# Optimization experiments

Hardware: AMD Instinct MI355X
Metric: run time of the kernel (lower is better)

The kernel has to match this reference:

```python
import jax, jax.numpy as jnp
import numpy as np

EPS = 1e-7  # keras K.epsilon()
ROUTINGS = 3


def squash(v, axis=-1):
    s = jnp.sum(v * v, axis=axis, keepdims=True)
    scale = s / (1.0 + s) / jnp.sqrt(s + EPS)
    return scale * v


def setup_inputs() -> dict:
    key = jax.random.key(0)
    k1, k2 = jax.random.split(key)
    B, I, K = 256, 2048, 8   # batch, input_num_capsule, input_dim_capsule
    J, D = 10, 16            # num_capsule, dim_capsule
    inputs = jax.random.normal(k1, (B, I, K), dtype=jnp.float32)
    W = jax.random.normal(k2, (J, I, D, K), dtype=jnp.float32) * 0.05
    return {"inputs": inputs, "W": W}


def reference(inputs, W):
    # inputs: [B, I, K]; W: [J, I, D, K]
    # inputs_hat[b,j,i,d] = W[j,i] @ inputs[b,i]  -> [B, J, I, D]
    u_hat = jnp.einsum('jidk,bik->bjid', W, inputs)
    B, J, I, _ = u_hat.shape
    b = jnp.zeros((B, J, 1, I), dtype=u_hat.dtype)
    outputs = None
    for r in range(ROUTINGS):
        c = jax.nn.softmax(b, axis=1)                       # softmax over output capsules
        s = jnp.einsum('bjqi,bjid->bjqd', c, u_hat)          # [B, J, 1, D]
        outputs = squash(s, axis=-1)
        if r < ROUTINGS - 1:
            b = b + jnp.einsum('bjqd,bjid->bjqi', outputs, u_hat)
    return jnp.squeeze(outputs, axis=2)                      # [B, J, D]
```

## Files before the change

### kernel.cpp

```cpp
#include <hip/hip_runtime.h>
#include <math.h>


#define BB 256
#define II 2048
#define KK 8
#define JJ 10
#define DD 16

typedef __attribute__((ext_vector_type(4))) float f32x4;
typedef __attribute__((ext_vector_type(8))) short short8;

__device__ __forceinline__ short f2bf(float f) {
    union { float f; unsigned u; } v; v.f = f;
    unsigned r = v.u + 0x7FFFu + ((v.u >> 16) & 1u);
    return (short)(r >> 16);
}

__global__ __launch_bounds__(256) void pre_kernel(const float* __restrict__ x,
                                                  const float* __restrict__ W,
                                                  short* __restrict__ xTb,
                                                  short* __restrict__ Wb) {
    __shared__ float4 tile[8 * 66];
    const int t = threadIdx.x;
    const int bid = blockIdx.x;
    if (bid < 1280) {
        const int idx = bid * 256 + t;
        const float4* src = (const float4*)(W + (size_t)idx * 8);
        const float4 a = src[0], b = src[1];
        short8 o;
        o[0] = f2bf(a.x); o[1] = f2bf(a.y); o[2] = f2bf(a.z); o[3] = f2bf(a.w);
        o[4] = f2bf(b.x); o[5] = f2bf(b.y); o[6] = f2bf(b.z); o[7] = f2bf(b.w);
        *(short8*)(Wb + (size_t)idx * 8) = o;
    } else {
        const int bb = bid - 1280;
        const int b0 = (bb >> 8) * 32, i0 = (bb & 255) * 8;
        {
            const int lb = t >> 3, li = t & 7;
            const float4* src = (const float4*)(x + ((b0 + lb) * II + (i0 + li)) * KK);
            tile[li * 66 + lb * 2 + 0] = src[0];
            tile[li * 66 + lb * 2 + 1] = src[1];
        }
        __syncthreads();
        {
            const int ri = t >> 5, rb = t & 31;
            const float4 p0 = tile[ri * 66 + rb * 2 + 0];
            const float4 p1 = tile[ri * 66 + rb * 2 + 1];
            short8 o;
            o[0] = f2bf(p0.x); o[1] = f2bf(p0.y); o[2] = f2bf(p0.z); o[3] = f2bf(p0.w);
            o[4] = f2bf(p1.x); o[5] = f2bf(p1.y); o[6] = f2bf(p1.z); o[7] = f2bf(p1.w);
            *(short8*)(xTb + ((size_t)(i0 + ri) * BB + (b0 + rb)) * KK) = o;
        }
    }
}

#define LBUF 14336

__device__ __forceinline__ void seg_src_dst(int s, int i0, int b0,
                                            const short* __restrict__ xTb,
                                            const short* __restrict__ Wb,
                                            const short** src, int* dst) {
    if (s < 20) {
        const int j = s >> 1, h = s & 1;
        *src = Wb + ((size_t)(j * II + i0) * DD) * KK + h * 512;
        *dst = j * 1024 + h * 512;
    } else {
        const int il = s - 20;
        *src = xTb + ((size_t)(i0 + il) * BB + b0) * KK;
        *dst = 10240 + il * 512;
    }
}

template <int USE_C>
__global__ __launch_bounds__(256) void round_mfma(
    const short* __restrict__ xTb, const short* __restrict__ Wb,
    const float* __restrict__ vT, _Float16* __restrict__ p)
{
    __shared__ short L[2][LBUF];
    const int t = threadIdx.x;
    const int lane = t & 63, wv = t >> 6;
    const int col = lane & 15, q = lane >> 4;
    const int b0 = blockIdx.y * 64;
    const int bl = wv * 16 + col;
    const int i0 = blockIdx.x * 16;

    short8 r0[7], r1[7];
#pragma unroll
    for (int n = 0; n < 7; ++n) {
        const int s = wv + n * 4;
        const short* src; int dst;
        seg_src_dst(s, i0, b0, xTb, Wb, &src, &dst);
        r0[n] = *(const short8*)(src + lane * 8);
        seg_src_dst(s, i0 + 8, b0, xTb, Wb, &src, &dst);
        r1[n] = *(const short8*)(src + lane * 8);
    }
#pragma unroll
    for (int n = 0; n < 7; ++n) {
        const int s = wv + n * 4;
        const short* src; int dst;
        seg_src_dst(s, i0, b0, xTb, Wb, &src, &dst);
        *(short8*)(&L[0][dst + lane * 8]) = r0[n];
    }
    __syncthreads();

    f32x4 sfrag[JJ];
#pragma unroll
    for (int j = 0; j < JJ; ++j) sfrag[j] = (f32x4){0.f, 0.f, 0.f, 0.f};

    float vfrag[JJ][4];
    if (USE_C) {
#pragma unroll
        for (int j = 0; j < JJ; ++j)
#pragma unroll
            for (int r = 0; r < 4; ++r)
                vfrag[j][r] = vT[(j * DD + q * 4 + r) * BB + b0 + bl];
    }

#pragma unroll
    for (int sc = 0; sc < 2; ++sc) {
        const short* Lb = L[sc];
        if (USE_C) {
            for (int il = 0; il < 8; ++il) {
                short8 A[JJ], Bf;
                const short8 z = (short8){0, 0, 0, 0, 0, 0, 0, 0};
                Bf = z;
#pragma unroll
                for (int j = 0; j < JJ; ++j) A[j] = z;
                if (q == 0) {
                    Bf = *(const short8*)(&Lb[10240 + il * 512 + bl * 8]);
#pragma unroll
                    for (int j = 0; j < JJ; ++j)
                        A[j] = *(const short8*)(&Lb[j * 1024 + il * 128 + col * 8]);
                }
                f32x4 U[JJ];
#pragma unroll
                for (int j = 0; j < JJ; ++j)
                    U[j] = __builtin_amdgcn_mfma_f32_16x16x32_bf16(
                        A[j], Bf, (f32x4){0.f, 0.f, 0.f, 0.f}, 0, 0, 0);
                float Lg[JJ];
#pragma unroll
                for (int j = 0; j < JJ; ++j)
                    Lg[j] = vfrag[j][0] * U[j][0] + vfrag[j][1] * U[j][1]
                          + vfrag[j][2] * U[j][2] + vfrag[j][3] * U[j][3];
#pragma unroll
                for (int j = 0; j < JJ; ++j) {
                    Lg[j] += __shfl_xor(Lg[j], 16, 64);
                    Lg[j] += __shfl_xor(Lg[j], 32, 64);
                }
                float sum = 0.f;
#pragma unroll
                for (int j = 0; j < JJ; ++j) { Lg[j] = __expf(Lg[j]); sum += Lg[j]; }
                const float inv = __builtin_amdgcn_rcpf(sum);
#pragma unroll
                for (int j = 0; j < JJ; ++j) {
                    const float c = Lg[j] * inv;
#pragma unroll
                    for (int r = 0; r < 4; ++r) sfrag[j][r] += c * U[j][r];
                }
            }
        } else {
#pragma unroll
            for (int s = 0; s < 2; ++s) {
                const int il = s * 4 + q;
                const short8 Bf = *(const short8*)(&Lb[10240 + il * 512 + bl * 8]);
#pragma unroll
                for (int j = 0; j < JJ; ++j) {
                    const short8 A = *(const short8*)(&Lb[j * 1024 + il * 128 + col * 8]);
                    sfrag[j] = __builtin_amdgcn_mfma_f32_16x16x32_bf16(A, Bf, sfrag[j], 0, 0, 0);
                }
            }
        }
        if (sc == 0) {
#pragma unroll
            for (int n = 0; n < 7; ++n) {
                const int s = wv + n * 4;
                const short* src; int dst;
                seg_src_dst(s, i0 + 8, b0, xTb, Wb, &src, &dst);
                *(short8*)(&L[1][dst + lane * 8]) = r1[n];
            }
            __syncthreads();
        }
    }

    _Float16* pp = p + ((size_t)(blockIdx.y * 4 + wv) * 128 + blockIdx.x) * (JJ * 256);
#pragma unroll
    for (int j = 0; j < JJ; ++j) {
        union { uint2 u; _Float16 h[4]; } pk;
        pk.h[0] = (_Float16)sfrag[j][0];
        pk.h[1] = (_Float16)sfrag[j][1];
        pk.h[2] = (_Float16)sfrag[j][2];
        pk.h[3] = (_Float16)sfrag[j][3];
        *(uint2*)(pp + (size_t)(j * 64 + lane) * 4) = pk.u;
    }
}

template <int MODE>
__global__ __launch_bounds__(256) void rs_kernel(const _Float16* __restrict__ p,
                                                 float* __restrict__ vT,
                                                 float* __restrict__ out, float scale) {
    __shared__ f32x4 red[256];
    const int t = threadIdx.x;
    const int j = blockIdx.x, bt = blockIdx.y;
    const int eg = t & 63, cg = t >> 6;

    const _Float16* pp = p + ((size_t)bt * 128 + cg * 32) * (JJ * 256) + j * 256 + eg * 4;
    float s0 = 0.f, s1 = 0.f, s2 = 0.f, s3 = 0.f;
#pragma unroll 8
    for (int ch = 0; ch < 32; ++ch) {
        union { uint2 u; _Float16 h[4]; } cv;
        cv.u = *(const uint2*)(pp + (size_t)ch * (JJ * 256));
        s0 += (float)cv.h[0]; s1 += (float)cv.h[1];
        s2 += (float)cv.h[2]; s3 += (float)cv.h[3];
    }
    red[t] = (f32x4){s0, s1, s2, s3};
    __syncthreads();
    if (t < 64) {
        f32x4 a = red[t];
        a += red[64 + t]; a += red[128 + t]; a += red[192 + t];
        const float x0 = a[0] * scale, x1 = a[1] * scale;
        const float x2 = a[2] * scale, x3 = a[3] * scale;
        float ss = x0 * x0 + x1 * x1 + x2 * x2 + x3 * x3;
        ss += __shfl_xor(ss, 16, 64);
        ss += __shfl_xor(ss, 32, 64);
        const float coef = ss / (1.f + ss) / sqrtf(ss + 1e-7f);
        const int qd = t >> 4, bc = t & 15;
        const float v[4] = {coef * x0, coef * x1, coef * x2, coef * x3};
#pragma unroll
        for (int r = 0; r < 4; ++r) {
            const int d = qd * 4 + r;
            if (MODE == 0) vT[(j * DD + d) * BB + bt * 16 + bc] = v[r];
            if (MODE == 1) vT[(j * DD + d) * BB + bt * 16 + bc] += v[r];
            if (MODE == 2) out[((bt * 16 + bc) * JJ + j) * DD + d] = v[r];
        }
    }
}

#define IT_OLD 32
#define BT_OLD 16

__global__ __launch_bounds__(256) void zero_kernel(float* __restrict__ p, int n) {
    int idx = blockIdx.x * blockDim.x + threadIdx.x;
    if (idx < n) p[idx] = 0.f;
}

__global__ __launch_bounds__(256) void squash_old(float* __restrict__ s_acc,
                                                  float* __restrict__ dst, float scale,
                                                  int add_to_dst, int zero_src) {
    int idx = blockIdx.x * blockDim.x + threadIdx.x;
    if (idx >= BB * JJ) return;
    float s[DD];
    float ss = 0.f;
#pragma unroll
    for (int d = 0; d < DD; ++d) {
        s[d] = s_acc[idx * DD + d] * scale;
        ss += s[d] * s[d];
    }
    const float coef = ss / (1.f + ss) / sqrtf(ss + 1e-7f);
#pragma unroll
    for (int d = 0; d < DD; ++d) {
        const float vv = coef * s[d];
        if (add_to_dst) dst[idx * DD + d] += vv;
        else            dst[idx * DD + d] = vv;
        if (zero_src)   s_acc[idx * DD + d] = 0.f;
    }
}

__global__ __launch_bounds__(256) void round1_old(const float* __restrict__ x,
                                                  const float* __restrict__ W,
                                                  float* __restrict__ s_acc) {
    const int t = threadIdx.x;
    const int d = t & 15;
    const int bq = t >> 4;
    const int b = blockIdx.y * BT_OLD + bq;
    const int i0 = blockIdx.x * IT_OLD;
    float acc[JJ];
#pragma unroll
    for (int j = 0; j < JJ; ++j) acc[j] = 0.f;
    for (int ii = 0; ii < IT_OLD; ++ii) {
        const int i = i0 + ii;
        const float* xp = x + ((b * II) + i) * KK;
        const float4 xa = *(const float4*)(xp);
        const float4 xb = *(const float4*)(xp + 4);
#pragma unroll
        for (int j = 0; j < JJ; ++j) {
            const float* wp = W + (((j * II + i) * DD + d) * KK);
            const float4 w0 = *(const float4*)(wp);
            const float4 w1 = *(const float4*)(wp + 4);
            acc[j] += w0.x*xa.x + w0.y*xa.y + w0.z*xa.z + w0.w*xa.w
                    + w1.x*xb.x + w1.y*xb.y + w1.z*xb.z + w1.w*xb.w;
        }
    }
#pragma unroll
    for (int j = 0; j < JJ; ++j)
        atomicAdd(&s_acc[(b * JJ + j) * DD + d], acc[j]);
}

__global__ __launch_bounds__(256) void round_old(const float* __restrict__ x,
                                                 const float* __restrict__ W,
                                                 const float* __restrict__ v,
                                                 float* __restrict__ s_acc) {
    const int t = threadIdx.x;
    const int d = t & 15;
    const int bq = t >> 4;
    const int b = blockIdx.y * BT_OLD + bq;
    const int i0 = blockIdx.x * IT_OLD;
    float vr[JJ], acc[JJ];
#pragma unroll
    for (int j = 0; j < JJ; ++j) {
        vr[j] = v[(b * JJ + j) * DD + d];
        acc[j] = 0.f;
    }
    for (int ii = 0; ii < IT_OLD; ++ii) {
        const int i = i0 + ii;
        const float* xp = x + ((b * II) + i) * KK;
        const float4 xa = *(const float4*)(xp);
        const float4 xb = *(const float4*)(xp + 4);
        float U[JJ], Lg[JJ];
#pragma unroll
        for (int j = 0; j < JJ; ++j) {
            const float* wp = W + (((j * II + i) * DD + d) * KK);
            const float4 w0 = *(const float4*)(wp);
            const float4 w1 = *(const float4*)(wp + 4);
            U[j] = w0.x*xa.x + w0.y*xa.y + w0.z*xa.z + w0.w*xa.w
                 + w1.x*xb.x + w1.y*xb.y + w1.z*xb.z + w1.w*xb.w;
            Lg[j] = vr[j] * U[j];
        }
#pragma unroll
        for (int m = 8; m >= 1; m >>= 1) {
#pragma unroll
            for (int j = 0; j < JJ; ++j) Lg[j] += __shfl_xor(Lg[j], m, 64);
        }
        float mx = Lg[0];
#pragma unroll
        for (int j = 1; j < JJ; ++j) mx = fmaxf(mx, Lg[j]);
        float sum = 0.f;
#pragma unroll
        for (int j = 0; j < JJ; ++j) { Lg[j] = __expf(Lg[j] - mx); sum += Lg[j]; }
        const float inv = 1.f / sum;
#pragma unroll
        for (int j = 0; j < JJ; ++j) acc[j] += (Lg[j] * inv) * U[j];
    }
#pragma unroll
    for (int j = 0; j < JJ; ++j)
        atomicAdd(&s_acc[(b * JJ + j) * DD + d], acc[j]);
}

extern "C" void kernel_launch(void* const* d_in, const int* in_sizes, int n_in,
                              void* d_out, int out_size, void* d_ws, size_t ws_size,
                              hipStream_t stream) {
    const float* x = (const float*)d_in[0];
    const float* W = (const float*)d_in[1];
    float* out = (float*)d_out;

    float* vT     = (float*)d_ws;
    _Float16* p   = (_Float16*)(vT + BB * JJ * DD);
    short* xTb    = (short*)(p + (size_t)16 * 128 * 2560);
    short* Wb     = xTb + (size_t)II * BB * KK;
    const size_t need = (size_t)(BB * JJ * DD) * 4
                      + (size_t)16 * 128 * 2560 * 2
                      + ((size_t)II * BB * KK + (size_t)JJ * II * DD * KK) * 2;

    if (ws_size >= need) {
        pre_kernel<<<1280 + 2048, 256, 0, stream>>>(x, W, xTb, Wb);

        dim3 rg(128, 4);
        dim3 sg(JJ, 16);
        round_mfma<0><<<rg, 256, 0, stream>>>(xTb, Wb, vT, p);
        rs_kernel<0><<<sg, 256, 0, stream>>>(p, vT, out, 0.1f);
        round_mfma<1><<<rg, 256, 0, stream>>>(xTb, Wb, vT, p);
        rs_kernel<1><<<sg, 256, 0, stream>>>(p, vT, out, 1.0f);
        round_mfma<1><<<rg, 256, 0, stream>>>(xTb, Wb, vT, p);
        rs_kernel<2><<<sg, 256, 0, stream>>>(p, vT, out, 1.0f);
    } else {
        float* s_acc = (float*)d_ws;
        float* v_buf = s_acc + BB * JJ * DD;
        const int NS = BB * JJ * DD;
        dim3 rg(II / IT_OLD, BB / BT_OLD);
        zero_kernel<<<(NS + 255) / 256, 256, 0, stream>>>(s_acc, NS);
        round1_old<<<rg, 256, 0, stream>>>(x, W, s_acc);
        squash_old<<<(BB * JJ + 255) / 256, 256, 0, stream>>>(s_acc, v_buf, 0.1f, 0, 1);
        round_old<<<rg, 256, 0, stream>>>(x, W, v_buf, s_acc);
        squash_old<<<(BB * JJ + 255) / 256, 256, 0, stream>>>(s_acc, v_buf, 1.0f, 1, 1);
        round_old<<<rg, 256, 0, stream>>>(x, W, v_buf, s_acc);
        squash_old<<<(BB * JJ + 255) / 256, 256, 0, stream>>>(s_acc, out, 1.0f, 0, 0);
    }
}
```

Measured before the change: 139.9 us.

## Double the input-capsule chunk per block with pipelined loads and packed partial sums

Each round_mfma block now covers 32 input capsules in four 8-capsule stages instead of 16 in two. Global loads for stage n+2 are issued while stage n is computed, and LDS buffers alternate between stages. Block IDs are remapped so that neighbouring blocks share W chunks across batch tiles. The partial-sum buffer is halved, its layout packs two output capsules per 16-byte store, and vT is changed to a [j][b][d] layout so it can be read with vector loads; rs_kernel is rewritten to match. The grid drops to 256 blocks, which lowers parallelism and may hurt occupancy across the GPU's compute units.

```diff
diff --git a/kernel.cpp b/kernel.cpp
--- a/kernel.cpp
+++ b/kernel.cpp
@@ -80,26 +80,29 @@
     const int t = threadIdx.x;
     const int lane = t & 63, wv = t >> 6;
     const int col = lane & 15, q = lane >> 4;
-    const int b0 = blockIdx.y * 64;
+    const int bid = blockIdx.x;
+    const int chunk = ((bid >> 5) << 3) | (bid & 7);
+    const int ytile = (bid >> 3) & 3;
+    const int b0 = ytile * 64;
     const int bl = wv * 16 + col;
-    const int i0 = blockIdx.x * 16;
-
-    short8 r0[7], r1[7];
+    const int i0 = chunk * 32;
+
+    short8 rA[7], rB[7];
 #pragma unroll
     for (int n = 0; n < 7; ++n) {
         const int s = wv + n * 4;
         const short* src; int dst;
         seg_src_dst(s, i0, b0, xTb, Wb, &src, &dst);
-        r0[n] = *(const short8*)(src + lane * 8);
+        rA[n] = *(const short8*)(src + lane * 8);
         seg_src_dst(s, i0 + 8, b0, xTb, Wb, &src, &dst);
-        r1[n] = *(const short8*)(src + lane * 8);
+        rB[n] = *(const short8*)(src + lane * 8);
     }
 #pragma unroll
     for (int n = 0; n < 7; ++n) {
         const int s = wv + n * 4;
         const short* src; int dst;
         seg_src_dst(s, i0, b0, xTb, Wb, &src, &dst);
-        *(short8*)(&L[0][dst + lane * 8]) = r0[n];
+        *(short8*)(&L[0][dst + lane * 8]) = rA[n];
     }
     __syncthreads();
 
@@ -107,18 +110,35 @@
 #pragma unroll
     for (int j = 0; j < JJ; ++j) sfrag[j] = (f32x4){0.f, 0.f, 0.f, 0.f};
 
-    float vfrag[JJ][4];
+    f32x4 vfrag[JJ];
     if (USE_C) {
 #pragma unroll
         for (int j = 0; j < JJ; ++j)
-#pragma unroll
-            for (int r = 0; r < 4; ++r)
-                vfrag[j][r] = vT[(j * DD + q * 4 + r) * BB + b0 + bl];
-    }
-
-#pragma unroll
-    for (int sc = 0; sc < 2; ++sc) {
-        const short* Lb = L[sc];
+            vfrag[j] = *(const f32x4*)(vT + ((size_t)j * BB + b0 + bl) * DD + q * 4);
+    }
+
+#pragma unroll
+    for (int sc = 0; sc < 4; ++sc) {
+        if (sc < 3) {
+#pragma unroll
+            for (int n = 0; n < 7; ++n) {
+                const int s = wv + n * 4;
+                const short* src; int dst;
+                seg_src_dst(s, i0 + (sc + 1) * 8, b0, xTb, Wb, &src, &dst);
+                *(short8*)(&L[(sc + 1) & 1][dst + lane * 8]) = (sc & 1) ? rA[n] : rB[n];
+            }
+        }
+        if (sc < 2) {
+#pragma unroll
+            for (int n = 0; n < 7; ++n) {
+                const int s = wv + n * 4;
+                const short* src; int dst;
+                seg_src_dst(s, i0 + (sc + 2) * 8, b0, xTb, Wb, &src, &dst);
+                if (sc & 1) rB[n] = *(const short8*)(src + lane * 8);
+                else        rA[n] = *(const short8*)(src + lane * 8);
+            }
+        }
+        const short* Lb = L[sc & 1];
         if (USE_C) {
             for (int il = 0; il < 8; ++il) {
                 short8 A[JJ], Bf;
@@ -170,27 +190,22 @@
                 }
             }
         }
-        if (sc == 0) {
-#pragma unroll
-            for (int n = 0; n < 7; ++n) {
-                const int s = wv + n * 4;
-                const short* src; int dst;
-                seg_src_dst(s, i0 + 8, b0, xTb, Wb, &src, &dst);
-                *(short8*)(&L[1][dst + lane * 8]) = r1[n];
-            }
-            __syncthreads();
-        }
-    }
-
-    _Float16* pp = p + ((size_t)(blockIdx.y * 4 + wv) * 128 + blockIdx.x) * (JJ * 256);
-#pragma unroll
-    for (int j = 0; j < JJ; ++j) {
-        union { uint2 u; _Float16 h[4]; } pk;
-        pk.h[0] = (_Float16)sfrag[j][0];
-        pk.h[1] = (_Float16)sfrag[j][1];
-        pk.h[2] = (_Float16)sfrag[j][2];
-        pk.h[3] = (_Float16)sfrag[j][3];
-        *(uint2*)(pp + (size_t)(j * 64 + lane) * 4) = pk.u;
+        if (sc < 3) __syncthreads();
+    }
+
+    _Float16* pp = p + (((size_t)(ytile * 4 + wv) * 64 + chunk) * 5) * 512;
+#pragma unroll
+    for (int jp = 0; jp < 5; ++jp) {
+        union { uint4 u; _Float16 h[8]; } pk;
+        pk.h[0] = (_Float16)sfrag[2 * jp][0];
+        pk.h[1] = (_Float16)sfrag[2 * jp][1];
+        pk.h[2] = (_Float16)sfrag[2 * jp][2];
+        pk.h[3] = (_Float16)sfrag[2 * jp][3];
+        pk.h[4] = (_Float16)sfrag[2 * jp + 1][0];
+        pk.h[5] = (_Float16)sfrag[2 * jp + 1][1];
+        pk.h[6] = (_Float16)sfrag[2 * jp + 1][2];
+        pk.h[7] = (_Float16)sfrag[2 * jp + 1][3];
+        *(uint4*)(pp + (size_t)(jp * 64 + lane) * 8) = pk.u;
     }
 }
 
@@ -198,39 +213,50 @@
 __global__ __launch_bounds__(256) void rs_kernel(const _Float16* __restrict__ p,
                                                  float* __restrict__ vT,
                                                  float* __restrict__ out, float scale) {
-    __shared__ f32x4 red[256];
+    __shared__ float red[256][9];
     const int t = threadIdx.x;
-    const int j = blockIdx.x, bt = blockIdx.y;
+    const int jp = blockIdx.x, bt = blockIdx.y;
     const int eg = t & 63, cg = t >> 6;
 
-    const _Float16* pp = p + ((size_t)bt * 128 + cg * 32) * (JJ * 256) + j * 256 + eg * 4;
-    float s0 = 0.f, s1 = 0.f, s2 = 0.f, s3 = 0.f;
-#pragma unroll 8
-    for (int ch = 0; ch < 32; ++ch) {
-        union { uint2 u; _Float16 h[4]; } cv;
-        cv.u = *(const uint2*)(pp + (size_t)ch * (JJ * 256));
-        s0 += (float)cv.h[0]; s1 += (float)cv.h[1];
-        s2 += (float)cv.h[2]; s3 += (float)cv.h[3];
-    }
-    red[t] = (f32x4){s0, s1, s2, s3};
+    const _Float16* pp = p + (((size_t)bt * 64 + cg * 16) * 5 + jp) * 512 + eg * 8;
+    float s[8];
+#pragma unroll
+    for (int r = 0; r < 8; ++r) s[r] = 0.f;
+#pragma unroll 4
+    for (int ch = 0; ch < 16; ++ch) {
+        union { uint4 u; _Float16 h[8]; } cv;
+        cv.u = *(const uint4*)(pp + (size_t)ch * (5 * 512));
+#pragma unroll
+        for (int r = 0; r < 8; ++r) s[r] += (float)cv.h[r];
+    }
+#pragma unroll
+    for (int r = 0; r < 8; ++r) red[t][r] = s[r];
     __syncthreads();
     if (t < 64) {
-        f32x4 a = red[t];
-        a += red[64 + t]; a += red[128 + t]; a += red[192 + t];
-        const float x0 = a[0] * scale, x1 = a[1] * scale;
-        const float x2 = a[2] * scale, x3 = a[3] * scale;
-        float ss = x0 * x0 + x1 * x1 + x2 * x2 + x3 * x3;
-        ss += __shfl_xor(ss, 16, 64);
-        ss += __shfl_xor(ss, 32, 64);
-        const float coef = ss / (1.f + ss) / sqrtf(ss + 1e-7f);
+        float a[8];
+#pragma unroll
+        for (int r = 0; r < 8; ++r)
+            a[r] = red[t][r] + red[t + 64][r] + red[t + 128][r] + red[t + 192][r];
         const int qd = t >> 4, bc = t & 15;
-        const float v[4] = {coef * x0, coef * x1, coef * x2, coef * x3};
-#pragma unroll
-        for (int r = 0; r < 4; ++r) {
-            const int d = qd * 4 + r;
-            if (MODE == 0) vT[(j * DD + d) * BB + bt * 16 + bc] = v[r];
-            if (MODE == 1) vT[(j * DD + d) * BB + bt * 16 + bc] += v[r];
-            if (MODE == 2) out[((bt * 16 + bc) * JJ + j) * DD + d] = v[r];
+#pragma unroll
+        for (int jj = 0; jj < 2; ++jj) {
+            const int j = jp * 2 + jj;
+            const float x0 = a[jj * 4 + 0] * scale, x1 = a[jj * 4 + 1] * scale;
+            const float x2 = a[jj * 4 + 2] * scale, x3 = a[jj * 4 + 3] * scale;
+            float ss = x0 * x0 + x1 * x1 + x2 * x2 + x3 * x3;
+            ss += __shfl_xor(ss, 16, 64);
+            ss += __shfl_xor(ss, 32, 64);
+            const float coef = ss / (1.f + ss) / sqrtf(ss + 1e-7f);
+            f32x4 v = {coef * x0, coef * x1, coef * x2, coef * x3};
+            if (MODE == 0)
+                *(f32x4*)(vT + ((size_t)j * BB + bt * 16 + bc) * DD + qd * 4) = v;
+            if (MODE == 1) {
+                f32x4 o = *(f32x4*)(vT + ((size_t)j * BB + bt * 16 + bc) * DD + qd * 4);
+                o += v;
+                *(f32x4*)(vT + ((size_t)j * BB + bt * 16 + bc) * DD + qd * 4) = o;
+            }
+            if (MODE == 2)
+                *(f32x4*)(out + ((size_t)(bt * 16 + bc) * JJ + j) * DD + qd * 4) = v;
         }
     }
 }
@@ -354,22 +380,21 @@
 
     float* vT     = (float*)d_ws;
     _Float16* p   = (_Float16*)(vT + BB * JJ * DD);
-    short* xTb    = (short*)(p + (size_t)16 * 128 * 2560);
+    short* xTb    = (short*)(p + (size_t)16 * 64 * 2560);
     short* Wb     = xTb + (size_t)II * BB * KK;
     const size_t need = (size_t)(BB * JJ * DD) * 4
-                      + (size_t)16 * 128 * 2560 * 2
+                      + (size_t)16 * 64 * 2560 * 2
                       + ((size_t)II * BB * KK + (size_t)JJ * II * DD * KK) * 2;
 
     if (ws_size >= need) {
         pre_kernel<<<1280 + 2048, 256, 0, stream>>>(x, W, xTb, Wb);
 
-        dim3 rg(128, 4);
-        dim3 sg(JJ, 16);
-        round_mfma<0><<<rg, 256, 0, stream>>>(xTb, Wb, vT, p);
+        dim3 sg(5, 16);
+        round_mfma<0><<<256, 256, 0, stream>>>(xTb, Wb, vT, p);
         rs_kernel<0><<<sg, 256, 0, stream>>>(p, vT, out, 0.1f);
-        round_mfma<1><<<rg, 256, 0, stream>>>(xTb, Wb, vT, p);
+        round_mfma<1><<<256, 256, 0, stream>>>(xTb, Wb, vT, p);
         rs_kernel<1><<<sg, 256, 0, stream>>>(p, vT, out, 1.0f);
-        round_mfma<1><<<rg, 256, 0, stream>>>(xTb, Wb, vT, p);
+        round_mfma<1><<<256, 256, 0, stream>>>(xTb, Wb, vT, p);
         rs_kernel<2><<<sg, 256, 0, stream>>>(p, vT, out, 1.0f);
     } else {
         float* s_acc = (float*)d_ws;
```

New measurement: 151.9 us. 8.6% more time.

## Fuse reduce-squash into round kernel via global atomic barrier

Applied to the files above, without the earlier changes.

Removes the separate rs_kernel launches by having every round_mfma block signal a global atomic counter after writing its partials. The first 160 blocks then spin until all 512 blocks have arrived and perform the reduction and squash in place. This cuts three kernel launches and their launch gaps. In exchange it relies on all 512 blocks being co-resident to avoid deadlock, adds a memset for the counters, and makes some blocks spin-wait.

```diff
diff --git a/kernel.cpp b/kernel.cpp
--- a/kernel.cpp
+++ b/kernel.cpp
@@ -71,18 +71,21 @@
     }
 }
 
-template <int USE_C>
+template <int USE_C, int MODE>
 __global__ __launch_bounds__(256) void round_mfma(
     const short* __restrict__ xTb, const short* __restrict__ Wb,
-    const float* __restrict__ vT, _Float16* __restrict__ p)
+    float* __restrict__ vT, _Float16* __restrict__ p, float* __restrict__ out,
+    unsigned* __restrict__ bar)
 {
     __shared__ short L[2][LBUF];
     const int t = threadIdx.x;
     const int lane = t & 63, wv = t >> 6;
     const int col = lane & 15, q = lane >> 4;
-    const int b0 = blockIdx.y * 64;
+    const int chunk = blockIdx.x;
+    const int ytile = blockIdx.y;
+    const int b0 = ytile * 64;
     const int bl = wv * 16 + col;
-    const int i0 = blockIdx.x * 16;
+    const int i0 = chunk * 16;
 
     short8 r0[7], r1[7];
 #pragma unroll
@@ -182,7 +185,7 @@
         }
     }
 
-    _Float16* pp = p + ((size_t)(blockIdx.y * 4 + wv) * 128 + blockIdx.x) * (JJ * 256);
+    _Float16* pp = p + ((size_t)(ytile * 4 + wv) * 128 + chunk) * (JJ * 256);
 #pragma unroll
     for (int j = 0; j < JJ; ++j) {
         union { uint2 u; _Float16 h[4]; } pk;
@@ -192,45 +195,59 @@
         pk.h[3] = (_Float16)sfrag[j][3];
         *(uint2*)(pp + (size_t)(j * 64 + lane) * 4) = pk.u;
     }
-}
-
-template <int MODE>
-__global__ __launch_bounds__(256) void rs_kernel(const _Float16* __restrict__ p,
-                                                 float* __restrict__ vT,
-                                                 float* __restrict__ out, float scale) {
-    __shared__ f32x4 red[256];
-    const int t = threadIdx.x;
-    const int j = blockIdx.x, bt = blockIdx.y;
-    const int eg = t & 63, cg = t >> 6;
-
-    const _Float16* pp = p + ((size_t)bt * 128 + cg * 32) * (JJ * 256) + j * 256 + eg * 4;
-    float s0 = 0.f, s1 = 0.f, s2 = 0.f, s3 = 0.f;
+
+    const int fbid = blockIdx.y * 128 + blockIdx.x;
+    __syncthreads();
+    if (t == 0) {
+        __threadfence();
+        __hip_atomic_fetch_add(&bar[MODE], 1u, __ATOMIC_RELEASE,
+                               __HIP_MEMORY_SCOPE_AGENT);
+    }
+    if (fbid >= JJ * 16) return;
+
+    if (t == 0) {
+        while (__hip_atomic_load(&bar[MODE], __ATOMIC_ACQUIRE,
+                                 __HIP_MEMORY_SCOPE_AGENT) < 512u)
+            __builtin_amdgcn_s_sleep(16);
+        __threadfence();
+    }
+    __syncthreads();
+
+    {
+        const int j = fbid >> 4, btq = fbid & 15;
+        const int eg = t & 63, cgi = t >> 6;
+        f32x4* red = (f32x4*)(&L[1][0]);
+        const _Float16* prd = p + ((size_t)btq * 128 + cgi * 32) * (JJ * 256)
+                            + j * 256 + eg * 4;
+        float s0 = 0.f, s1 = 0.f, s2 = 0.f, s3 = 0.f;
 #pragma unroll 8
-    for (int ch = 0; ch < 32; ++ch) {
-        union { uint2 u; _Float16 h[4]; } cv;
-        cv.u = *(const uint2*)(pp + (size_t)ch * (JJ * 256));
-        s0 += (float)cv.h[0]; s1 += (float)cv.h[1];
-        s2 += (float)cv.h[2]; s3 += (float)cv.h[3];
-    }
-    red[t] = (f32x4){s0, s1, s2, s3};
-    __syncthreads();
-    if (t < 64) {
-        f32x4 a = red[t];
-        a += red[64 + t]; a += red[128 + t]; a += red[192 + t];
-        const float x0 = a[0] * scale, x1 = a[1] * scale;
-        const float x2 = a[2] * scale, x3 = a[3] * scale;
-        float ss = x0 * x0 + x1 * x1 + x2 * x2 + x3 * x3;
-        ss += __shfl_xor(ss, 16, 64);
-        ss += __shfl_xor(ss, 32, 64);
-        const float coef = ss / (1.f + ss) / sqrtf(ss + 1e-7f);
-        const int qd = t >> 4, bc = t & 15;
-        const float v[4] = {coef * x0, coef * x1, coef * x2, coef * x3};
-#pragma unroll
-        for (int r = 0; r < 4; ++r) {
-            const int d = qd * 4 + r;
-            if (MODE == 0) vT[(j * DD + d) * BB + bt * 16 + bc] = v[r];
-            if (MODE == 1) vT[(j * DD + d) * BB + bt * 16 + bc] += v[r];
-            if (MODE == 2) out[((bt * 16 + bc) * JJ + j) * DD + d] = v[r];
+        for (int ch = 0; ch < 32; ++ch) {
+            union { uint2 u; _Float16 h[4]; } cv;
+            cv.u = *(const uint2*)(prd + (size_t)ch * (JJ * 256));
+            s0 += (float)cv.h[0]; s1 += (float)cv.h[1];
+            s2 += (float)cv.h[2]; s3 += (float)cv.h[3];
+        }
+        red[t] = (f32x4){s0, s1, s2, s3};
+        __syncthreads();
+        if (t < 64) {
+            f32x4 a = red[t];
+            a += red[64 + t]; a += red[128 + t]; a += red[192 + t];
+            const float scale = (MODE == 0) ? 0.1f : 1.0f;
+            const float x0 = a[0] * scale, x1 = a[1] * scale;
+            const float x2 = a[2] * scale, x3 = a[3] * scale;
+            float ss = x0 * x0 + x1 * x1 + x2 * x2 + x3 * x3;
+            ss += __shfl_xor(ss, 16, 64);
+            ss += __shfl_xor(ss, 32, 64);
+            const float coef = ss / (1.f + ss) / sqrtf(ss + 1e-7f);
+            const int qd = t >> 4, bc = t & 15;
+            const float v[4] = {coef * x0, coef * x1, coef * x2, coef * x3};
+#pragma unroll
+            for (int r = 0; r < 4; ++r) {
+                const int d = qd * 4 + r;
+                if (MODE == 0) vT[(j * DD + d) * BB + btq * 16 + bc] = v[r];
+                if (MODE == 1) vT[(j * DD + d) * BB + btq * 16 + bc] += v[r];
+                if (MODE == 2) out[((btq * 16 + bc) * JJ + j) * DD + d] = v[r];
+            }
         }
     }
 }
@@ -352,25 +369,23 @@
     const float* W = (const float*)d_in[1];
     float* out = (float*)d_out;
 
-    float* vT     = (float*)d_ws;
+    unsigned* bar = (unsigned*)d_ws;
+    float* vT     = (float*)((char*)d_ws + 64);
     _Float16* p   = (_Float16*)(vT + BB * JJ * DD);
     short* xTb    = (short*)(p + (size_t)16 * 128 * 2560);
     short* Wb     = xTb + (size_t)II * BB * KK;
-    const size_t need = (size_t)(BB * JJ * DD) * 4
+    const size_t need = 64 + (size_t)(BB * JJ * DD) * 4
                       + (size_t)16 * 128 * 2560 * 2
                       + ((size_t)II * BB * KK + (size_t)JJ * II * DD * KK) * 2;
 
     if (ws_size >= need) {
+        hipMemsetAsync(bar, 0, 64, stream);
         pre_kernel<<<1280 + 2048, 256, 0, stream>>>(x, W, xTb, Wb);
 
         dim3 rg(128, 4);
-        dim3 sg(JJ, 16);
-        round_mfma<0><<<rg, 256, 0, stream>>>(xTb, Wb, vT, p);
-        rs_kernel<0><<<sg, 256, 0, stream>>>(p, vT, out, 0.1f);
-        round_mfma<1><<<rg, 256, 0, stream>>>(xTb, Wb, vT, p);
-        rs_kernel<1><<<sg, 256, 0, stream>>>(p, vT, out, 1.0f);
-        round_mfma<1><<<rg, 256, 0, stream>>>(xTb, Wb, vT, p);
-        rs_kernel<2><<<sg, 256, 0, stream>>>(p, vT, out, 1.0f);
+        round_mfma<0, 0><<<rg, 256, 0, stream>>>(xTb, Wb, vT, p, out, bar);
+        round_mfma<1, 1><<<rg, 256, 0, stream>>>(xTb, Wb, vT, p, out, bar);
+        round_mfma<1, 2><<<rg, 256, 0, stream>>>(xTb, Wb, vT, p, out, bar);
     } else {
         float* s_acc = (float*)d_ws;
         float* v_buf = s_acc + BB * JJ * DD;
```

Measured after the change: 268.1 us. 1.92x slower.
